# Optimization experiments

Measured on AMD Instinct MI355X. Metric: run time of the kernel, lower is better.

## Reference

```python
import jax, jax.numpy as jnp
import numpy as np

B, S, F, H = 64, 1024, 64, 128


def setup_inputs() -> dict:
    key = jax.random.key(0)
    ks = jax.random.split(key, 12)
    s = 1.0 / np.sqrt(H)
    u = lambda k, shape: jax.random.uniform(k, shape, jnp.float32, -s, s)
    return {
        "x": jax.random.normal(ks[0], (B, S, F), jnp.float32),
        "mu": jax.random.normal(ks[1], (B, 1, F), jnp.float32),
        "W_ih0": u(ks[2], (4 * H, F)),
        "W_hh0": u(ks[3], (4 * H, H)),
        "b_ih0": u(ks[4], (4 * H,)),
        "b_hh0": u(ks[5], (4 * H,)),
        "W_ih1": u(ks[6], (4 * H, H)),
        "W_hh1": u(ks[7], (4 * H, H)),
        "b_ih1": u(ks[8], (4 * H,)),
        "b_hh1": u(ks[9], (4 * H,)),
        "fc_w": u(ks[10], (1, H)),
        "fc_b": u(ks[11], (1,)),
    }


def _cell(x_gates, h, c, Whh, bias):
    # PyTorch LSTM cell: gates ordered i, f, g, o
    g = x_gates + h @ Whh.T + bias
    i, f, gg, o = jnp.split(g, 4, axis=-1)
    c = jax.nn.sigmoid(f) * c + jax.nn.sigmoid(i) * jnp.tanh(gg)
    h = jax.nn.sigmoid(o) * jnp.tanh(c)
    return h, c


def _lstm2(x1, x2, Wih, Whh, bih, bhh):
    # 2-step LSTM layer from zero initial state; returns per-step hidden states
    bias = bih + bhh
    n = x1.shape[0]
    hd = Whh.shape[1]
    h0 = jnp.zeros((n, hd), x1.dtype)
    h1, c1 = _cell(x1 @ Wih.T, h0, h0, Whh, bias)
    h2, _ = _cell(x2 @ Wih.T, h1, c1, Whh, bias)
    return h1, h2


def reference(x, mu, W_ih0, W_hh0, b_ih0, b_hh0, W_ih1, W_hh1, b_ih1, b_hh1, fc_w, fc_b):
    b, s, f = x.shape
    # Every timestep runs an independent 2-step LSTM [x_t, mu] from zero state,
    # so fold (batch, seq) into one big batch of B*S instances.
    x1 = x.reshape(b * s, f)                                   # step-1 inputs
    x2 = jnp.broadcast_to(mu, (b, s, f)).reshape(b * s, f)     # step-2 inputs (mu)
    h1, h2 = _lstm2(x1, x2, W_ih0, W_hh0, b_ih0, b_hh0)        # layer 0
    _, h2 = _lstm2(h1, h2, W_ih1, W_hh1, b_ih1, b_hh1)         # layer 1
    h = jax.nn.relu(h2).reshape(b, s, -1)                      # relu; dropout is identity (eval)
    out = h @ fc_w.T + fc_b                                    # [B, S, 1]
    return out
```

## Files before the change

### kernel.cpp

```cpp
#include <hip/hip_runtime.h>


typedef _Float16 half8 __attribute__((ext_vector_type(8)));
typedef _Float16 half4_t __attribute__((ext_vector_type(4)));
typedef float f32x4 __attribute__((ext_vector_type(4)));

#define L2E  1.4426950408889634f
#define L2E2 2.8853900817779268f

#define WP_WIH0 0
#define WP_WHH0 32768
#define WP_WIH1 98304
#define WP_WHH1 163840
#define WS_BIAS0 458752
#define WS_BIAS1 (458752 + 2048)
#define WS_MUG2  (458752 + 4096)

__global__ void prep_kernel(const float* __restrict__ Wih0,
                            const float* __restrict__ Whh0,
                            const float* __restrict__ Wih1,
                            const float* __restrict__ Whh1,
                            const float* __restrict__ bih0,
                            const float* __restrict__ bhh0,
                            const float* __restrict__ bih1,
                            const float* __restrict__ bhh1,
                            const float* __restrict__ mu,
                            _Float16* __restrict__ Wp,
                            float* __restrict__ bias0f,
                            float* __restrict__ bias1f,
                            float* __restrict__ mu_g2)
{
    int blk = blockIdx.x;
    if (blk >= 113) {
        int o = (blk - 113) * 256 + threadIdx.x;
        int b = o >> 9;
        int n = o & 511;
        float s = bih0[n] + bhh0[n];
        const float* m = mu + b * 64;
        const float* wrow = Wih0 + n * 64;
        #pragma unroll 8
        for (int k = 0; k < 64; ++k) s += m[k] * wrow[k];
        float scale = ((n >> 7) == 2) ? L2E2 : L2E;
        mu_g2[o] = s * scale;
        return;
    }
    if (blk == 112) {
        int i = threadIdx.x;
        float sc_hi = (i < 128) ? L2E2 : L2E;
        bias0f[i]       = (bih0[i]       + bhh0[i])       * L2E;
        bias0f[i + 256] = (bih0[i + 256] + bhh0[i + 256]) * sc_hi;
        bias1f[i]       = (bih1[i]       + bhh1[i])       * L2E;
        bias1f[i + 256] = (bih1[i + 256] + bhh1[i + 256]) * sc_hi;
        return;
    }
    int gidx = blk * 256 + threadIdx.x;
    const float* src; int KC, Kw, local;
    if (gidx < 4096)       { src = Wih0; KC = 2; Kw = 64;  local = gidx; }
    else if (gidx < 12288) { src = Whh0; KC = 4; Kw = 128; local = gidx - 4096; }
    else if (gidx < 20480) { src = Wih1; KC = 4; Kw = 128; local = gidx - 12288; }
    else                   { src = Whh1; KC = 4; Kw = 128; local = gidx - 20480; }
    int lane = local & 63;
    int tmp  = local >> 6;
    int kc   = tmp % KC;
    int nt   = tmp / KC;
    int n  = nt * 16 + (lane & 15);
    int k0 = kc * 32 + (lane >> 4) * 8;
    float scale = ((n >> 7) == 2) ? L2E2 : L2E;
    const float* s = src + n * Kw + k0;
    half8 hv;
    #pragma unroll
    for (int j = 0; j < 8; ++j) hv[j] = (_Float16)(s[j] * scale);
    *(half8*)(Wp + (size_t)gidx * 8) = hv;
}

__device__ __forceinline__ float sig2(float a) {
    return __builtin_amdgcn_rcpf(1.0f + __builtin_amdgcn_exp2f(-a));
}
__device__ __forceinline__ float tanh2(float a) {
    return fmaf(-2.0f, __builtin_amdgcn_rcpf(1.0f + __builtin_amdgcn_exp2f(a)), 1.0f);
}

template<int KC>
__device__ __forceinline__ void gemm_stage(const _Float16* __restrict__ Wp,
                                           const _Float16* A, const int strideA,
                                           int w, int lane, f32x4 acc[4][4])
{
    const int c = lane & 15, q = lane >> 4;
    #pragma unroll
    for (int kc = 0; kc < KC; ++kc) {
        half8 a[4], bq[4];
        #pragma unroll
        for (int mt = 0; mt < 4; ++mt)
            a[mt] = *(const half8*)(A + (mt * 16 + c) * strideA + kc * 32 + q * 8);
        #pragma unroll
        for (int g = 0; g < 4; ++g)
            bq[g] = *(const half8*)(Wp + (((g * 8 + w) * KC + kc) * 64 + lane) * 8);
        #pragma unroll
        for (int mt = 0; mt < 4; ++mt)
            #pragma unroll
            for (int g = 0; g < 4; ++g)
                acc[mt][g] = __builtin_amdgcn_mfma_f32_16x16x32_f16(bq[g], a[mt], acc[mt][g], 0, 0, 0);
    }
}

__global__ __launch_bounds__(512) void lstm_main(
    const float* __restrict__ x, const _Float16* __restrict__ Wp_in,
    const float* __restrict__ bias0f_in, const float* __restrict__ bias1f_in,
    const float* __restrict__ mu_g2_in, const float* __restrict__ fc_w_in,
    const float* __restrict__ fc_b_in, float* __restrict__ out)
{
    __shared__ __align__(16) char smem[70656];
    _Float16* H1s  = (_Float16*)(smem);
    _Float16* H2s  = (_Float16*)(smem + 17408);
    _Float16* H11s = (_Float16*)(smem + 34816);

    const int t = threadIdx.x;
    const int w = t >> 6, lane = t & 63, c = lane & 15, q = lane >> 4;
    const int wg = blockIdx.x;
    const int b = wg >> 3;

    const int jbase = w * 16 + q * 4;
    const int bq_idx = w * 4 + q;

    {
        const float* xp = x + (size_t)wg * 8192 + t * 8;
        float4 u0 = ((const float4*)xp)[0];
        float4 u1 = ((const float4*)xp)[1];
        half8 hv;
        hv[0] = (_Float16)u0.x; hv[1] = (_Float16)u0.y;
        hv[2] = (_Float16)u0.z; hv[3] = (_Float16)u0.w;
        hv[4] = (_Float16)u1.x; hv[5] = (_Float16)u1.y;
        hv[6] = (_Float16)u1.z; hv[7] = (_Float16)u1.w;
        *(half8*)((_Float16*)(smem + 52224) + (t >> 3) * 72 + (t & 7) * 8) = hv;
        if (t < 128) out[(size_t)wg * 128 + t] = fc_b_in[0];
    }
    __syncthreads();

    for (int tile = 0; tile < 2; ++tile) {
        const _Float16* Wp   = Wp_in;
        const float* bias0f  = bias0f_in;
        const float* bias1f  = bias1f_in;
        const float* mu_g2b  = mu_g2_in + b * 512;
        const float* fc_w    = fc_w_in;
        asm volatile("" : "+v"(Wp), "+v"(bias0f), "+v"(bias1f),
                          "+v"(mu_g2b), "+v"(fc_w));

        const _Float16* A0 = (const _Float16*)(smem + 52224 + tile * 9216);

        f32x4 acc[4][4];
        float cc[4][4];

        #pragma unroll
        for (int g = 0; g < 4; ++g) {
            f32x4 bv = ((const f32x4*)bias0f)[g * 32 + bq_idx];
            #pragma unroll
            for (int mt = 0; mt < 4; ++mt) acc[mt][g] = bv;
        }
        gemm_stage<2>(Wp + WP_WIH0, A0, 72, w, lane, acc);

        if (tile == 0) {
            const float* xp = x + (size_t)wg * 8192 + 4096 + t * 8;
            float4 u0 = ((const float4*)xp)[0];
            float4 u1 = ((const float4*)xp)[1];
            half8 hv;
            hv[0] = (_Float16)u0.x; hv[1] = (_Float16)u0.y;
            hv[2] = (_Float16)u0.z; hv[3] = (_Float16)u0.w;
            hv[4] = (_Float16)u1.x; hv[5] = (_Float16)u1.y;
            hv[6] = (_Float16)u1.z; hv[7] = (_Float16)u1.w;
            *(half8*)((_Float16*)(smem + 61440) + (t >> 3) * 72 + (t & 7) * 8) = hv;
        }

        #pragma unroll
        for (int mt = 0; mt < 4; ++mt) {
            half4_t hv;
            #pragma unroll
            for (int r = 0; r < 4; ++r) {
                float c1 = sig2(acc[mt][0][r]) * tanh2(acc[mt][2][r]);
                cc[mt][r] = c1;
                hv[r] = (_Float16)(sig2(acc[mt][3][r]) * tanh2(c1 * L2E2));
            }
            *(half4_t*)(H1s + (mt * 16 + c) * 136 + jbase) = hv;
        }
        __syncthreads();

        #pragma unroll
        for (int g = 0; g < 4; ++g) {
            f32x4 bv = ((const f32x4*)mu_g2b)[g * 32 + bq_idx];
            #pragma unroll
            for (int mt = 0; mt < 4; ++mt) acc[mt][g] = bv;
        }
        gemm_stage<4>(Wp + WP_WHH0, H1s, 136, w, lane, acc);
        #pragma unroll
        for (int mt = 0; mt < 4; ++mt) {
            half4_t hv;
            #pragma unroll
            for (int r = 0; r < 4; ++r) {
                float c2 = sig2(acc[mt][1][r]) * cc[mt][r]
                         + sig2(acc[mt][0][r]) * tanh2(acc[mt][2][r]);
                hv[r] = (_Float16)(sig2(acc[mt][3][r]) * tanh2(c2 * L2E2));
            }
            *(half4_t*)(H2s + (mt * 16 + c) * 136 + jbase) = hv;
        }

        #pragma unroll
        for (int g = 0; g < 4; ++g) {
            f32x4 bv = ((const f32x4*)bias1f)[g * 32 + bq_idx];
            #pragma unroll
            for (int mt = 0; mt < 4; ++mt) acc[mt][g] = bv;
        }
        gemm_stage<4>(Wp + WP_WIH1, H1s, 136, w, lane, acc);
        #pragma unroll
        for (int mt = 0; mt < 4; ++mt) {
            half4_t hv;
            #pragma unroll
            for (int r = 0; r < 4; ++r) {
                float c1 = sig2(acc[mt][0][r]) * tanh2(acc[mt][2][r]);
                cc[mt][r] = c1;
                hv[r] = (_Float16)(sig2(acc[mt][3][r]) * tanh2(c1 * L2E2));
            }
            *(half4_t*)(H11s + (mt * 16 + c) * 136 + jbase) = hv;
        }
        __syncthreads();

        #pragma unroll
        for (int g = 0; g < 4; ++g) {
            f32x4 bv = ((const f32x4*)bias1f)[g * 32 + bq_idx];
            #pragma unroll
            for (int mt = 0; mt < 4; ++mt) acc[mt][g] = bv;
        }
        gemm_stage<4>(Wp + WP_WIH1, H2s, 136, w, lane, acc);
        gemm_stage<4>(Wp + WP_WHH1, H11s, 136, w, lane, acc);

        {
            f32x4 fwv = ((const f32x4*)fc_w)[bq_idx];
            #pragma unroll
            for (int mt = 0; mt < 4; ++mt) {
                float v = 0.0f;
                #pragma unroll
                for (int r = 0; r < 4; ++r) {
                    float c2 = sig2(acc[mt][1][r]) * cc[mt][r]
                             + sig2(acc[mt][0][r]) * tanh2(acc[mt][2][r]);
                    float h  = sig2(acc[mt][3][r]) * tanh2(c2 * L2E2);
                    v = fmaf(fmaxf(h, 0.0f), fwv[r], v);
                }
                v += __shfl_xor(v, 16);
                v += __shfl_xor(v, 32);
                if (lane < 16)
                    atomicAdd(out + (size_t)wg * 128 + tile * 64 + mt * 16 + lane, v);
            }
        }
    }
}

extern "C" void kernel_launch(void* const* d_in, const int* in_sizes, int n_in,
                              void* d_out, int out_size, void* d_ws, size_t ws_size,
                              hipStream_t stream)
{
    const float* x    = (const float*)d_in[0];
    const float* mu   = (const float*)d_in[1];
    const float* Wih0 = (const float*)d_in[2];
    const float* Whh0 = (const float*)d_in[3];
    const float* bih0 = (const float*)d_in[4];
    const float* bhh0 = (const float*)d_in[5];
    const float* Wih1 = (const float*)d_in[6];
    const float* Whh1 = (const float*)d_in[7];
    const float* bih1 = (const float*)d_in[8];
    const float* bhh1 = (const float*)d_in[9];
    const float* fcw  = (const float*)d_in[10];
    const float* fcb  = (const float*)d_in[11];
    float* out = (float*)d_out;

    _Float16* Wp  = (_Float16*)d_ws;
    float* bias0f = (float*)((char*)d_ws + WS_BIAS0);
    float* bias1f = (float*)((char*)d_ws + WS_BIAS1);
    float* mu_g2  = (float*)((char*)d_ws + WS_MUG2);

    hipLaunchKernelGGL(prep_kernel, dim3(241), dim3(256), 0, stream,
                       Wih0, Whh0, Wih1, Whh1, bih0, bhh0, bih1, bhh1, mu,
                       Wp, bias0f, bias1f, mu_g2);
    hipLaunchKernelGGL(lstm_main, dim3(512), dim3(512), 0, stream,
                       x, Wp, bias0f, bias1f, mu_g2, fcw, fcb, out);
}
```

Baseline: 143.9 us.

## Split blocks to 64 rows, swizzle LDS, load x to registers, interleave stages

Each block now handles 64 rows instead of two 128-row tiles, doubling the grid to 1024 blocks and cutting shared memory to 48KB with launch bounds requesting more resident blocks per CU. LDS hidden-state buffers use an XOR swizzle instead of padded strides to avoid bank conflicts. Input x is loaded straight into registers as MFMA operands, and weight pointers are pinned as scalars. The layer-1 first-step GEMM is interleaved per row tile with the H2 activation, and s_setprio raises wave priority around MFMA sections. In exchange, the weight fetches are repeated across twice as many blocks and register pressure rises under the tighter occupancy target.

```diff
diff --git a/kernel.cpp b/kernel.cpp
--- a/kernel.cpp
+++ b/kernel.cpp
@@ -80,10 +80,14 @@
     return fmaf(-2.0f, __builtin_amdgcn_rcpf(1.0f + __builtin_amdgcn_exp2f(a)), 1.0f);
 }
 
+__device__ __forceinline__ int swz(int row, int col) {
+    return (row << 8) + (col ^ ((row & 7) << 4));
+}
+
 template<int KC>
-__device__ __forceinline__ void gemm_stage(const _Float16* __restrict__ Wp,
-                                           const _Float16* A, const int strideA,
-                                           int w, int lane, f32x4 acc[4][4])
+__device__ __forceinline__ void gemm_lds(const _Float16* __restrict__ Wq,
+                                         const char* Hb,
+                                         int w, int lane, f32x4 acc[4][4])
 {
     const int c = lane & 15, q = lane >> 4;
     #pragma unroll
@@ -91,10 +95,10 @@
         half8 a[4], bq[4];
         #pragma unroll
         for (int mt = 0; mt < 4; ++mt)
-            a[mt] = *(const half8*)(A + (mt * 16 + c) * strideA + kc * 32 + q * 8);
+            a[mt] = *(const half8*)(Hb + swz(mt * 16 + c, kc * 64 + q * 16));
         #pragma unroll
         for (int g = 0; g < 4; ++g)
-            bq[g] = *(const half8*)(Wp + (((g * 8 + w) * KC + kc) * 64 + lane) * 8);
+            bq[g] = *(const half8*)(Wq + (((g * 8 + w) * KC + kc) * 64 + lane) * 8);
         #pragma unroll
         for (int mt = 0; mt < 4; ++mt)
             #pragma unroll
@@ -103,93 +107,111 @@
     }
 }
 
-__global__ __launch_bounds__(512) void lstm_main(
+__global__ __launch_bounds__(512, 4) void lstm_main(
     const float* __restrict__ x, const _Float16* __restrict__ Wp_in,
     const float* __restrict__ bias0f_in, const float* __restrict__ bias1f_in,
     const float* __restrict__ mu_g2_in, const float* __restrict__ fc_w_in,
     const float* __restrict__ fc_b_in, float* __restrict__ out)
 {
-    __shared__ __align__(16) char smem[70656];
-    _Float16* H1s  = (_Float16*)(smem);
-    _Float16* H2s  = (_Float16*)(smem + 17408);
-    _Float16* H11s = (_Float16*)(smem + 34816);
+    __shared__ __align__(16) char smem[49152];
+    char* H1s  = smem;
+    char* H2s  = smem + 16384;
+    char* H11s = smem + 32768;
 
     const int t = threadIdx.x;
     const int w = t >> 6, lane = t & 63, c = lane & 15, q = lane >> 4;
     const int wg = blockIdx.x;
-    const int b = wg >> 3;
-
-    const int jbase = w * 16 + q * 4;
+    const int b = wg >> 4;
     const int bq_idx = w * 4 + q;
 
-    {
-        const float* xp = x + (size_t)wg * 8192 + t * 8;
-        float4 u0 = ((const float4*)xp)[0];
-        float4 u1 = ((const float4*)xp)[1];
-        half8 hv;
-        hv[0] = (_Float16)u0.x; hv[1] = (_Float16)u0.y;
-        hv[2] = (_Float16)u0.z; hv[3] = (_Float16)u0.w;
-        hv[4] = (_Float16)u1.x; hv[5] = (_Float16)u1.y;
-        hv[6] = (_Float16)u1.z; hv[7] = (_Float16)u1.w;
-        *(half8*)((_Float16*)(smem + 52224) + (t >> 3) * 72 + (t & 7) * 8) = hv;
-        if (t < 128) out[(size_t)wg * 128 + t] = fc_b_in[0];
-    }
-    __syncthreads();
-
-    for (int tile = 0; tile < 2; ++tile) {
-        const _Float16* Wp   = Wp_in;
-        const float* bias0f  = bias0f_in;
-        const float* bias1f  = bias1f_in;
-        const float* mu_g2b  = mu_g2_in + b * 512;
-        const float* fc_w    = fc_w_in;
-        asm volatile("" : "+v"(Wp), "+v"(bias0f), "+v"(bias1f),
-                          "+v"(mu_g2b), "+v"(fc_w));
-
-        const _Float16* A0 = (const _Float16*)(smem + 52224 + tile * 9216);
-
-        f32x4 acc[4][4];
-        float cc[4][4];
-
+    half8 ax[8];
+    {
+        const float* xb = x + (size_t)wg * 4096;
+        #pragma unroll
+        for (int mt = 0; mt < 4; ++mt)
+            #pragma unroll
+            for (int kc = 0; kc < 2; ++kc) {
+                const float* p = xb + (mt * 16 + c) * 64 + kc * 32 + q * 8;
+                float4 u0 = ((const float4*)p)[0];
+                float4 u1 = ((const float4*)p)[1];
+                half8 hv;
+                hv[0] = (_Float16)u0.x; hv[1] = (_Float16)u0.y;
+                hv[2] = (_Float16)u0.z; hv[3] = (_Float16)u0.w;
+                hv[4] = (_Float16)u1.x; hv[5] = (_Float16)u1.y;
+                hv[6] = (_Float16)u1.z; hv[7] = (_Float16)u1.w;
+                ax[mt * 2 + kc] = hv;
+            }
+        if (t < 64) out[(size_t)wg * 64 + t] = fc_b_in[0];
+    }
+
+    f32x4 acc[4][4];
+    float cc[4][4];
+
+    {
+        const float* bias0f = bias0f_in; asm volatile("" : "+s"(bias0f));
         #pragma unroll
         for (int g = 0; g < 4; ++g) {
             f32x4 bv = ((const f32x4*)bias0f)[g * 32 + bq_idx];
             #pragma unroll
             for (int mt = 0; mt < 4; ++mt) acc[mt][g] = bv;
         }
-        gemm_stage<2>(Wp + WP_WIH0, A0, 72, w, lane, acc);
-
-        if (tile == 0) {
-            const float* xp = x + (size_t)wg * 8192 + 4096 + t * 8;
-            float4 u0 = ((const float4*)xp)[0];
-            float4 u1 = ((const float4*)xp)[1];
-            half8 hv;
-            hv[0] = (_Float16)u0.x; hv[1] = (_Float16)u0.y;
-            hv[2] = (_Float16)u0.z; hv[3] = (_Float16)u0.w;
-            hv[4] = (_Float16)u1.x; hv[5] = (_Float16)u1.y;
-            hv[6] = (_Float16)u1.z; hv[7] = (_Float16)u1.w;
-            *(half8*)((_Float16*)(smem + 61440) + (t >> 3) * 72 + (t & 7) * 8) = hv;
-        }
-
-        #pragma unroll
-        for (int mt = 0; mt < 4; ++mt) {
-            half4_t hv;
-            #pragma unroll
-            for (int r = 0; r < 4; ++r) {
-                float c1 = sig2(acc[mt][0][r]) * tanh2(acc[mt][2][r]);
-                cc[mt][r] = c1;
-                hv[r] = (_Float16)(sig2(acc[mt][3][r]) * tanh2(c1 * L2E2));
-            }
-            *(half4_t*)(H1s + (mt * 16 + c) * 136 + jbase) = hv;
-        }
-        __syncthreads();
-
+    }
+    {
+        const _Float16* W0 = Wp_in + WP_WIH0; asm volatile("" : "+s"(W0));
+        __builtin_amdgcn_s_setprio(1);
+        #pragma unroll
+        for (int kc = 0; kc < 2; ++kc) {
+            half8 bq[4];
+            #pragma unroll
+            for (int g = 0; g < 4; ++g)
+                bq[g] = *(const half8*)(W0 + (((g * 8 + w) * 2 + kc) * 64 + lane) * 8);
+            #pragma unroll
+            for (int mt = 0; mt < 4; ++mt)
+                #pragma unroll
+                for (int g = 0; g < 4; ++g)
+                    acc[mt][g] = __builtin_amdgcn_mfma_f32_16x16x32_f16(bq[g], ax[mt * 2 + kc], acc[mt][g], 0, 0, 0);
+        }
+        __builtin_amdgcn_s_setprio(0);
+    }
+    #pragma unroll
+    for (int mt = 0; mt < 4; ++mt) {
+        half4_t hv;
+        #pragma unroll
+        for (int r = 0; r < 4; ++r) {
+            float c1 = sig2(acc[mt][0][r]) * tanh2(acc[mt][2][r]);
+            cc[mt][r] = c1;
+            hv[r] = (_Float16)(sig2(acc[mt][3][r]) * tanh2(c1 * L2E2));
+        }
+        *(half4_t*)(H1s + swz(mt * 16 + c, w * 32 + q * 8)) = hv;
+    }
+    __syncthreads();
+
+    {
+        const float* mu_g2b = mu_g2_in + b * 512; asm volatile("" : "+s"(mu_g2b));
         #pragma unroll
         for (int g = 0; g < 4; ++g) {
             f32x4 bv = ((const f32x4*)mu_g2b)[g * 32 + bq_idx];
             #pragma unroll
             for (int mt = 0; mt < 4; ++mt) acc[mt][g] = bv;
         }
-        gemm_stage<4>(Wp + WP_WHH0, H1s, 136, w, lane, acc);
+    }
+    {
+        const _Float16* Wq = Wp_in + WP_WHH0; asm volatile("" : "+s"(Wq));
+        __builtin_amdgcn_s_setprio(1);
+        gemm_lds<4>(Wq, H1s, w, lane, acc);
+        __builtin_amdgcn_s_setprio(0);
+    }
+
+    f32x4 bv1[4];
+    {
+        const float* bias1f = bias1f_in; asm volatile("" : "+s"(bias1f));
+        #pragma unroll
+        for (int g = 0; g < 4; ++g)
+            bv1[g] = ((const f32x4*)bias1f)[g * 32 + bq_idx];
+    }
+
+    {
+        const _Float16* Wih1p = Wp_in + WP_WIH1; asm volatile("" : "+s"(Wih1p));
         #pragma unroll
         for (int mt = 0; mt < 4; ++mt) {
             half4_t hv;
@@ -199,55 +221,64 @@
                          + sig2(acc[mt][0][r]) * tanh2(acc[mt][2][r]);
                 hv[r] = (_Float16)(sig2(acc[mt][3][r]) * tanh2(c2 * L2E2));
             }
-            *(half4_t*)(H2s + (mt * 16 + c) * 136 + jbase) = hv;
-        }
-
-        #pragma unroll
-        for (int g = 0; g < 4; ++g) {
-            f32x4 bv = ((const f32x4*)bias1f)[g * 32 + bq_idx];
-            #pragma unroll
-            for (int mt = 0; mt < 4; ++mt) acc[mt][g] = bv;
-        }
-        gemm_stage<4>(Wp + WP_WIH1, H1s, 136, w, lane, acc);
+            *(half4_t*)(H2s + swz(mt * 16 + c, w * 32 + q * 8)) = hv;
+            #pragma unroll
+            for (int g = 0; g < 4; ++g) acc[mt][g] = bv1[g];
+            __builtin_amdgcn_s_setprio(1);
+            #pragma unroll
+            for (int kc = 0; kc < 4; ++kc) {
+                half8 av = *(const half8*)(H1s + swz(mt * 16 + c, kc * 64 + q * 16));
+                #pragma unroll
+                for (int g = 0; g < 4; ++g) {
+                    half8 bq = *(const half8*)(Wih1p + (((g * 8 + w) * 4 + kc) * 64 + lane) * 8);
+                    acc[mt][g] = __builtin_amdgcn_mfma_f32_16x16x32_f16(bq, av, acc[mt][g], 0, 0, 0);
+                }
+            }
+            __builtin_amdgcn_s_setprio(0);
+        }
+    }
+    #pragma unroll
+    for (int mt = 0; mt < 4; ++mt) {
+        half4_t hv;
+        #pragma unroll
+        for (int r = 0; r < 4; ++r) {
+            float c1 = sig2(acc[mt][0][r]) * tanh2(acc[mt][2][r]);
+            cc[mt][r] = c1;
+            hv[r] = (_Float16)(sig2(acc[mt][3][r]) * tanh2(c1 * L2E2));
+        }
+        *(half4_t*)(H11s + swz(mt * 16 + c, w * 32 + q * 8)) = hv;
+    }
+    __syncthreads();
+
+    #pragma unroll
+    for (int g = 0; g < 4; ++g)
+        #pragma unroll
+        for (int mt = 0; mt < 4; ++mt) acc[mt][g] = bv1[g];
+    {
+        const _Float16* Wa = Wp_in + WP_WIH1; asm volatile("" : "+s"(Wa));
+        const _Float16* Wb = Wp_in + WP_WHH1; asm volatile("" : "+s"(Wb));
+        __builtin_amdgcn_s_setprio(1);
+        gemm_lds<4>(Wa, H2s,  w, lane, acc);
+        gemm_lds<4>(Wb, H11s, w, lane, acc);
+        __builtin_amdgcn_s_setprio(0);
+    }
+    {
+        const float* fc_w = fc_w_in; asm volatile("" : "+s"(fc_w));
+        f32x4 fwv = ((const f32x4*)fc_w)[bq_idx];
         #pragma unroll
         for (int mt = 0; mt < 4; ++mt) {
-            half4_t hv;
+            float v = 0.0f;
             #pragma unroll
             for (int r = 0; r < 4; ++r) {
-                float c1 = sig2(acc[mt][0][r]) * tanh2(acc[mt][2][r]);
-                cc[mt][r] = c1;
-                hv[r] = (_Float16)(sig2(acc[mt][3][r]) * tanh2(c1 * L2E2));
+                float c2 = sig2(acc[mt][1][r]) * cc[mt][r]
+                         + sig2(acc[mt][0][r]) * tanh2(acc[mt][2][r]);
+                float h  = sig2(acc[mt][3][r]) * tanh2(c2 * L2E2);
+                v = fmaf(fmaxf(h, 0.0f), fwv[r], v);
             }
-            *(half4_t*)(H11s + (mt * 16 + c) * 136 + jbase) = hv;
-        }
-        __syncthreads();
-
-        #pragma unroll
-        for (int g = 0; g < 4; ++g) {
-            f32x4 bv = ((const f32x4*)bias1f)[g * 32 + bq_idx];
-            #pragma unroll
-            for (int mt = 0; mt < 4; ++mt) acc[mt][g] = bv;
-        }
-        gemm_stage<4>(Wp + WP_WIH1, H2s, 136, w, lane, acc);
-        gemm_stage<4>(Wp + WP_WHH1, H11s, 136, w, lane, acc);
-
-        {
-            f32x4 fwv = ((const f32x4*)fc_w)[bq_idx];
-            #pragma unroll
-            for (int mt = 0; mt < 4; ++mt) {
-                float v = 0.0f;
-                #pragma unroll
-                for (int r = 0; r < 4; ++r) {
-                    float c2 = sig2(acc[mt][1][r]) * cc[mt][r]
-                             + sig2(acc[mt][0][r]) * tanh2(acc[mt][2][r]);
-                    float h  = sig2(acc[mt][3][r]) * tanh2(c2 * L2E2);
-                    v = fmaf(fmaxf(h, 0.0f), fwv[r], v);
-                }
-                v += __shfl_xor(v, 16);
-                v += __shfl_xor(v, 32);
-                if (lane < 16)
-                    atomicAdd(out + (size_t)wg * 128 + tile * 64 + mt * 16 + lane, v);
-            }
+            v += __shfl_xor(v, 16);
+            v += __shfl_xor(v, 32);
+            if (lane < 16)
+                atomicAdd(out + (size_t)wg * 64 + mt * 16 + lane, v);
         }
     }
 }
@@ -278,6 +309,6 @@
     hipLaunchKernelGGL(prep_kernel, dim3(241), dim3(256), 0, stream,
                        Wih0, Whh0, Wih1, Whh1, bih0, bhh0, bih1, bhh1, mu,
                        Wp, bias0f, bias1f, mu_g2);
-    hipLaunchKernelGGL(lstm_main, dim3(512), dim3(512), 0, stream,
+    hipLaunchKernelGGL(lstm_main, dim3(1024), dim3(512), 0, stream,
                        x, Wp, bias0f, bias1f, mu_g2, fcw, fcb, out);
 }
```

New measurement: 173.7 us. 20.7% more time.
